# Kernel optimization log

Hardware: AMD Instinct MI355X
Metric: run time of the kernel (lower is better)

The kernel has to match this reference:

```python
import jax, jax.numpy as jnp
import numpy as np

WINDOW = 128
LOOK_BACKWARD = 1
LOOK_FORWARD = 0
DIM_HEAD = 64
ROPE_BASE = 10000.0


def look_around(x, backward=LOOK_BACKWARD, forward=LOOK_FORWARD, pad_value=-1):
    # x: [b, w, n, ...] -> pad window axis, gather shifted windows, concat along n axis
    w = x.shape[1]
    pads = [(0, 0)] * x.ndim
    pads[1] = (backward, forward)
    padded = jnp.pad(x, pads, constant_values=pad_value)
    return jnp.concatenate([padded[:, i:i + w] for i in range(backward + forward + 1)], axis=2)


def _rotate_half(x):
    x1, x2 = jnp.split(x, 2, axis=-1)
    return jnp.concatenate([-x2, x1], axis=-1)


def apply_rotary(bq, bk):
    # sinusoidal embeddings computed over the look-around key length j; queries use the last n positions
    j = bk.shape[2]
    n = bq.shape[2]
    inv_freq = 1.0 / (ROPE_BASE ** (jnp.arange(0, DIM_HEAD, 2, dtype=jnp.float32) / DIM_HEAD))
    t = jnp.arange(j, dtype=jnp.float32)
    freqs = t[:, None] * inv_freq[None, :]          # [j, d/2]
    freqs = jnp.concatenate([freqs, freqs], axis=-1)  # [j, d]
    q_freqs = freqs[-n:]
    bq = bq * jnp.cos(q_freqs) + _rotate_half(bq) * jnp.sin(q_freqs)
    bk = bk * jnp.cos(freqs) + _rotate_half(bk) * jnp.sin(freqs)
    return bq, bk


def setup_inputs() -> dict:
    key = jax.random.key(0)
    kq, kk, kv = jax.random.split(key, 3)
    shape = (4, 8, 4096, 64)
    return {
        'q': jax.random.normal(kq, shape, dtype=jnp.float32),
        'k': jax.random.normal(kk, shape, dtype=jnp.float32),
        'v': jax.random.normal(kv, shape, dtype=jnp.float32),
    }


def reference(q, k, v):
    B, H, N, D = q.shape
    b = B * H
    q_ = q.reshape(b, N, D)
    k_ = k.reshape(b, N, D)
    v_ = v.reshape(b, N, D)
    w = N // WINDOW
    scale = D ** -0.5

    seq = jnp.arange(N)
    b_t = seq.reshape(1, w, WINDOW)                           # [1, w, n]

    bq = q_.reshape(b, w, WINDOW, D) * scale
    bk = look_around(k_.reshape(b, w, WINDOW, D), pad_value=-1.0)  # [b, w, j, d]
    bv = look_around(v_.reshape(b, w, WINDOW, D), pad_value=-1.0)

    bq, bk = apply_rotary(bq, bk)

    bq_t = b_t[..., :, None]                                  # [1, w, n, 1]
    bq_k = look_around(b_t, pad_value=-1)[..., None, :]        # [1, w, 1, j]
    pad_mask = bq_k == -1
    causal_mask = bq_t < bq_k

    sim = jnp.einsum('bwie,bwje->bwij', bq, bk)                # [b, w, n, j]
    mask_value = -jnp.finfo(sim.dtype).max
    sim = jnp.where(causal_mask | pad_mask, mask_value, sim)

    attn = jax.nn.softmax(sim, axis=-1)
    out = jnp.einsum('bwij,bwje->bwie', attn, bv)
    return out.reshape(B, H, N, D)
```

## Files before the change

kernel.cpp:

```cpp
#include <hip/hip_runtime.h>
#include <hip/hip_bf16.h>
#include <float.h>

typedef __attribute__((ext_vector_type(8))) _Float16 f16x8;
typedef __attribute__((ext_vector_type(4))) _Float16 f16x4;
typedef __attribute__((ext_vector_type(4))) float f32x4;

#define WIN 128
#define KEYS 256
#define DH 64
#define NWIN 32
#define SEQ 4096
#define QS 72
#define KSTR 72
#define VSTR 264
#define PSTR 136
#define L2B_OVER 0.41524101186092156f

__launch_bounds__(512, 1)
__global__ void lattn_kernel(const float* __restrict__ q,
                             const float* __restrict__ k,
                             const float* __restrict__ v,
                             float* __restrict__ out) {
  __shared__ __align__(16) _Float16 qsm[WIN * QS];
  __shared__ __align__(16) _Float16 ksm[KEYS * KSTR];
  __shared__ __align__(16) _Float16 vsm[DH * VSTR];
  __shared__ __align__(16) _Float16 psm[8 * 16 * PSTR];

  const int bid  = blockIdx.x;
  const int bh   = bid >> 5;
  const int win  = bid & 31;
  const int tid  = threadIdx.x;
  const int wv   = tid >> 6;
  const int lane = tid & 63;
  const int c    = lane & 15;
  const int g    = lane >> 4;

  const float* qb = q + ((size_t)bh * SEQ + (size_t)win * WIN) * DH;

  #pragma unroll
  for (int it = 0; it < 2; ++it) {
    int item = it * 512 + tid;
    int row = item >> 3, p = item & 7;
    const float4* src = (const float4*)(qb + row * DH);
    float4 lo = src[p];
    float4 hi = src[p + 8];
    float pos = (float)(128 + row);
    f16x4 rl, rh;
    #pragma unroll
    for (int j = 0; j < 4; ++j) {
      float invf = exp2f(-(float)(4 * p + j) * L2B_OVER);
      float sn, cs;
      __sincosf(pos * invf, &sn, &cs);
      float x = ((const float*)&lo)[j];
      float y = ((const float*)&hi)[j];
      rl[j] = (_Float16)((x * cs - y * sn) * 0.125f);
      rh[j] = (_Float16)((y * cs + x * sn) * 0.125f);
    }
    *(f16x4*)(&qsm[row * QS + 4 * p])      = rl;
    *(f16x4*)(&qsm[row * QS + 4 * p + 32]) = rh;
  }

  #pragma unroll
  for (int it = 0; it < 4; ++it) {
    int item = it * 512 + tid;
    int row = item >> 3, p = item & 7;
    long grow = (long)win * WIN - WIN + row;
    float4 lo = {0.f, 0.f, 0.f, 0.f}, hi = {0.f, 0.f, 0.f, 0.f};
    if (grow >= 0) {
      const float4* src = (const float4*)(k + ((size_t)bh * SEQ + grow) * DH);
      lo = src[p];
      hi = src[p + 8];
    }
    float pos = (float)row;
    f16x4 rl, rh;
    #pragma unroll
    for (int j = 0; j < 4; ++j) {
      float invf = exp2f(-(float)(4 * p + j) * L2B_OVER);
      float sn, cs;
      __sincosf(pos * invf, &sn, &cs);
      float x = ((const float*)&lo)[j];
      float y = ((const float*)&hi)[j];
      rl[j] = (_Float16)(x * cs - y * sn);
      rh[j] = (_Float16)(y * cs + x * sn);
    }
    *(f16x4*)(&ksm[row * KSTR + 4 * p])      = rl;
    *(f16x4*)(&ksm[row * KSTR + 4 * p + 32]) = rh;
  }

  #pragma unroll
  for (int it = 0; it < 8; ++it) {
    int item = it * 512 + tid;
    int row = item >> 4, p = item & 15;
    long grow = (long)win * WIN - WIN + row;
    float4 val = {0.f, 0.f, 0.f, 0.f};
    if (grow >= 0)
      val = *(const float4*)(v + ((size_t)bh * SEQ + grow) * DH + 4 * p);
    #pragma unroll
    for (int i = 0; i < 4; ++i)
      vsm[(4 * p + i) * VSTR + row] = (_Float16)(((const float*)&val)[i]);
  }

  __syncthreads();

  f16x8 qf[2];
  #pragma unroll
  for (int ks = 0; ks < 2; ++ks)
    qf[ks] = *(const f16x8*)(&qsm[(16 * wv + c) * QS + 32 * ks + 8 * g]);

  f32x4 acc[16];
  #pragma unroll
  for (int mt = 0; mt < 16; ++mt) acc[mt] = (f32x4){0.f, 0.f, 0.f, 0.f};

  #pragma unroll
  for (int mt = 0; mt < 16; ++mt) {
    #pragma unroll
    for (int ks = 0; ks < 2; ++ks) {
      f16x8 kf = *(const f16x8*)(&ksm[(16 * mt + c) * KSTR + 32 * ks + 8 * g]);
      acc[mt] = __builtin_amdgcn_mfma_f32_16x16x32_f16(kf, qf[ks], acc[mt], 0, 0, 0);
    }
  }

  const int qi   = 16 * wv + c;
  const int kmin = (win == 0) ? 128 : 0;
  float m = -FLT_MAX;
  #pragma unroll
  for (int mt = 0; mt < 16; ++mt) {
    #pragma unroll
    for (int r = 0; r < 4; ++r) {
      int j = 16 * mt + 4 * g + r;
      bool ok = (j <= qi + 128) && (j >= kmin);
      float s = ok ? acc[mt][r] : -FLT_MAX;
      acc[mt][r] = s;
      m = fmaxf(m, s);
    }
  }
  m = fmaxf(m, __shfl_xor(m, 16));
  m = fmaxf(m, __shfl_xor(m, 32));

  float sm = 0.f;
  #pragma unroll
  for (int mt = 0; mt < 16; ++mt) {
    #pragma unroll
    for (int r = 0; r < 4; ++r) {
      float p = __expf(acc[mt][r] - m);
      acc[mt][r] = p;
      sm += p;
    }
  }
  sm += __shfl_xor(sm, 16);
  sm += __shfl_xor(sm, 32);
  const float rinv = 1.0f / sm;

  f32x4 oacc[4];
  #pragma unroll
  for (int nt = 0; nt < 4; ++nt) oacc[nt] = (f32x4){0.f, 0.f, 0.f, 0.f};

  _Float16* pw = &psm[wv * 16 * PSTR];

  #pragma unroll
  for (int h = 0; h < 2; ++h) {
    if (h) {
      asm volatile("s_waitcnt lgkmcnt(0)" ::: "memory");
      __builtin_amdgcn_sched_barrier(0);
    }
    #pragma unroll
    for (int mt8 = 0; mt8 < 8; ++mt8) {
      int mt = 8 * h + mt8;
      f16x4 pv4;
      #pragma unroll
      for (int r = 0; r < 4; ++r) pv4[r] = (_Float16)(acc[mt][r] * rinv);
      *(f16x4*)(&pw[c * PSTR + 16 * mt8 + 4 * g]) = pv4;
    }
    asm volatile("s_waitcnt lgkmcnt(0)" ::: "memory");
    __builtin_amdgcn_sched_barrier(0);

    #pragma unroll
    for (int ks = 0; ks < 4; ++ks) {
      f16x8 pf = *(const f16x8*)(&pw[c * PSTR + 32 * ks + 8 * g]);
      #pragma unroll
      for (int nt = 0; nt < 4; ++nt) {
        f16x8 vf = *(const f16x8*)(&vsm[(16 * nt + c) * VSTR + 128 * h + 32 * ks + 8 * g]);
        oacc[nt] = __builtin_amdgcn_mfma_f32_16x16x32_f16(pf, vf, oacc[nt], 0, 0, 0);
      }
    }
  }

  float* ob = out + ((size_t)bh * SEQ + (size_t)win * WIN + 16 * wv) * DH;
  #pragma unroll
  for (int nt = 0; nt < 4; ++nt) {
    #pragma unroll
    for (int r = 0; r < 4; ++r) {
      ob[(4 * g + r) * DH + 16 * nt + c] = oacc[nt][r];
    }
  }
}

extern "C" void kernel_launch(void* const* d_in, const int* in_sizes, int n_in,
                              void* d_out, int out_size, void* d_ws, size_t ws_size,
                              hipStream_t stream) {
  const float* q = (const float*)d_in[0];
  const float* k = (const float*)d_in[1];
  const float* v = (const float*)d_in[2];
  float* out = (float*)d_out;
  dim3 grid(32 * 32);
  lattn_kernel<<<grid, 512, 0, stream>>>(q, k, v, out);
}
```

Baseline: 51.01 us.

## Load and rotate Q in registers, alias P over K in LDS, remap blocks

Q is now loaded straight into per-lane registers and rotated there, so the Q shared-memory tile and its LDS round trip are gone. The softmax probability buffer reuses the K tile's LDS space, with an extra barrier before the first write. This cuts LDS to about 69KB per block, and launch bounds are raised to allow more blocks per CU. Block IDs are remapped to interleave (batch·head, window) pairs, and the K/V load indexing is rearranged. The cost is an extra __syncthreads and possible register pressure under the higher occupancy target.

After: 43.34 us. 15.0% less time.

```diff
diff --git a/kernel.cpp b/kernel.cpp
--- a/kernel.cpp
+++ b/kernel.cpp
@@ -1,5 +1,4 @@
 #include <hip/hip_runtime.h>
-#include <hip/hip_bf16.h>
 #include <float.h>
 
 typedef __attribute__((ext_vector_type(8))) _Float16 f16x8;
@@ -7,80 +6,61 @@
 typedef __attribute__((ext_vector_type(4))) float f32x4;
 
 #define WIN 128
-#define KEYS 256
+#define SEQ 4096
 #define DH 64
-#define NWIN 32
-#define SEQ 4096
-#define QS 72
 #define KSTR 72
 #define VSTR 264
 #define PSTR 136
+#define VOFF 36864
 #define L2B_OVER 0.41524101186092156f
 
-__launch_bounds__(512, 1)
+__launch_bounds__(512, 4)
 __global__ void lattn_kernel(const float* __restrict__ q,
                              const float* __restrict__ k,
                              const float* __restrict__ v,
                              float* __restrict__ out) {
-  __shared__ __align__(16) _Float16 qsm[WIN * QS];
-  __shared__ __align__(16) _Float16 ksm[KEYS * KSTR];
-  __shared__ __align__(16) _Float16 vsm[DH * VSTR];
-  __shared__ __align__(16) _Float16 psm[8 * 16 * PSTR];
+  __shared__ __align__(16) char smem[70656];
+  _Float16* ksm = (_Float16*)smem;
+  _Float16* psm = (_Float16*)smem;
+  _Float16* vsm = (_Float16*)(smem + VOFF);
 
   const int bid  = blockIdx.x;
-  const int bh   = bid >> 5;
-  const int win  = bid & 31;
+  const int lbid = (bid & 7) * 128 + (bid >> 3);
+  const int bh   = lbid >> 5;
+  const int win  = lbid & 31;
   const int tid  = threadIdx.x;
   const int wv   = tid >> 6;
   const int lane = tid & 63;
   const int c    = lane & 15;
   const int g    = lane >> 4;
 
-  const float* qb = q + ((size_t)bh * SEQ + (size_t)win * WIN) * DH;
-
-  #pragma unroll
-  for (int it = 0; it < 2; ++it) {
-    int item = it * 512 + tid;
-    int row = item >> 3, p = item & 7;
-    const float4* src = (const float4*)(qb + row * DH);
-    float4 lo = src[p];
-    float4 hi = src[p + 8];
-    float pos = (float)(128 + row);
-    f16x4 rl, rh;
-    #pragma unroll
-    for (int j = 0; j < 4; ++j) {
-      float invf = exp2f(-(float)(4 * p + j) * L2B_OVER);
-      float sn, cs;
-      __sincosf(pos * invf, &sn, &cs);
-      float x = ((const float*)&lo)[j];
-      float y = ((const float*)&hi)[j];
-      rl[j] = (_Float16)((x * cs - y * sn) * 0.125f);
-      rh[j] = (_Float16)((y * cs + x * sn) * 0.125f);
-    }
-    *(f16x4*)(&qsm[row * QS + 4 * p])      = rl;
-    *(f16x4*)(&qsm[row * QS + 4 * p + 32]) = rh;
-  }
+  const int qrow = 16 * wv + c;
+  const float* qp = q + ((size_t)bh * SEQ + (size_t)win * WIN + qrow) * DH;
+  const float4 x0 = *(const float4*)(qp + 8 * g);
+  const float4 x1 = *(const float4*)(qp + 8 * g + 4);
+  const float4 y0 = *(const float4*)(qp + 8 * g + 32);
+  const float4 y1 = *(const float4*)(qp + 8 * g + 36);
 
   #pragma unroll
   for (int it = 0; it < 4; ++it) {
-    int item = it * 512 + tid;
-    int row = item >> 3, p = item & 7;
+    int hi  = it * 8 + wv;
+    int row = c + 16 * (hi >> 1);
+    int p   = g + 4 * (hi & 1);
     long grow = (long)win * WIN - WIN + row;
-    float4 lo = {0.f, 0.f, 0.f, 0.f}, hi = {0.f, 0.f, 0.f, 0.f};
+    float4 lo = {0.f, 0.f, 0.f, 0.f}, hi4 = {0.f, 0.f, 0.f, 0.f};
     if (grow >= 0) {
       const float4* src = (const float4*)(k + ((size_t)bh * SEQ + grow) * DH);
-      lo = src[p];
-      hi = src[p + 8];
+      lo  = src[p];
+      hi4 = src[p + 8];
     }
     float pos = (float)row;
     f16x4 rl, rh;
     #pragma unroll
     for (int j = 0; j < 4; ++j) {
-      float invf = exp2f(-(float)(4 * p + j) * L2B_OVER);
       float sn, cs;
-      __sincosf(pos * invf, &sn, &cs);
+      __sincosf(pos * exp2f(-(float)(4 * p + j) * L2B_OVER), &sn, &cs);
       float x = ((const float*)&lo)[j];
-      float y = ((const float*)&hi)[j];
+      float y = ((const float*)&hi4)[j];
       rl[j] = (_Float16)(x * cs - y * sn);
       rh[j] = (_Float16)(y * cs + x * sn);
     }
@@ -90,38 +70,50 @@
 
   #pragma unroll
   for (int it = 0; it < 8; ++it) {
-    int item = it * 512 + tid;
-    int row = item >> 4, p = item & 15;
+    int hi  = it * 8 + wv;
+    int row = c + 16 * (hi & 15);
+    int pf  = g + 4 * (hi >> 4);
     long grow = (long)win * WIN - WIN + row;
     float4 val = {0.f, 0.f, 0.f, 0.f};
     if (grow >= 0)
-      val = *(const float4*)(v + ((size_t)bh * SEQ + grow) * DH + 4 * p);
+      val = *(const float4*)(v + ((size_t)bh * SEQ + grow) * DH + 4 * pf);
     #pragma unroll
     for (int i = 0; i < 4; ++i)
-      vsm[(4 * p + i) * VSTR + row] = (_Float16)(((const float*)&val)[i]);
+      vsm[(4 * pf + i) * VSTR + row] = (_Float16)(((const float*)&val)[i]);
+  }
+
+  f16x8 qf0, qf1;
+  {
+    float pos = (float)(128 + qrow);
+    #pragma unroll
+    for (int j = 0; j < 4; ++j) {
+      float sn, cs;
+      __sincosf(pos * exp2f(-(float)(8 * g + j) * L2B_OVER), &sn, &cs);
+      float xa = ((const float*)&x0)[j], ya = ((const float*)&y0)[j];
+      qf0[j]     = (_Float16)((xa * cs - ya * sn) * 0.125f);
+      qf1[j]     = (_Float16)((ya * cs + xa * sn) * 0.125f);
+      __sincosf(pos * exp2f(-(float)(8 * g + 4 + j) * L2B_OVER), &sn, &cs);
+      float xb = ((const float*)&x1)[j], yb = ((const float*)&y1)[j];
+      qf0[4 + j] = (_Float16)((xb * cs - yb * sn) * 0.125f);
+      qf1[4 + j] = (_Float16)((yb * cs + xb * sn) * 0.125f);
+    }
   }
 
   __syncthreads();
 
-  f16x8 qf[2];
-  #pragma unroll
-  for (int ks = 0; ks < 2; ++ks)
-    qf[ks] = *(const f16x8*)(&qsm[(16 * wv + c) * QS + 32 * ks + 8 * g]);
-
   f32x4 acc[16];
   #pragma unroll
   for (int mt = 0; mt < 16; ++mt) acc[mt] = (f32x4){0.f, 0.f, 0.f, 0.f};
 
   #pragma unroll
   for (int mt = 0; mt < 16; ++mt) {
-    #pragma unroll
-    for (int ks = 0; ks < 2; ++ks) {
-      f16x8 kf = *(const f16x8*)(&ksm[(16 * mt + c) * KSTR + 32 * ks + 8 * g]);
-      acc[mt] = __builtin_amdgcn_mfma_f32_16x16x32_f16(kf, qf[ks], acc[mt], 0, 0, 0);
-    }
-  }
-
-  const int qi   = 16 * wv + c;
+    f16x8 kf0 = *(const f16x8*)(&ksm[(16 * mt + c) * KSTR + 8 * g]);
+    f16x8 kf1 = *(const f16x8*)(&ksm[(16 * mt + c) * KSTR + 32 + 8 * g]);
+    acc[mt] = __builtin_amdgcn_mfma_f32_16x16x32_f16(kf0, qf0, acc[mt], 0, 0, 0);
+    acc[mt] = __builtin_amdgcn_mfma_f32_16x16x32_f16(kf1, qf1, acc[mt], 0, 0, 0);
+  }
+
+  const int qi   = qrow;
   const int kmin = (win == 0) ? 128 : 0;
   float m = -FLT_MAX;
   #pragma unroll
@@ -152,11 +144,13 @@
   sm += __shfl_xor(sm, 32);
   const float rinv = 1.0f / sm;
 
+  __syncthreads();
+
   f32x4 oacc[4];
   #pragma unroll
   for (int nt = 0; nt < 4; ++nt) oacc[nt] = (f32x4){0.f, 0.f, 0.f, 0.f};
 
-  _Float16* pw = &psm[wv * 16 * PSTR];
+  _Float16* pw = psm + wv * 16 * PSTR;
 
   #pragma unroll
   for (int h = 0; h < 2; ++h) {
```
